# Optimization experiments

Measured on AMD Instinct MI355X. Metric: run time of the kernel, lower is better.

The kernel has to match this reference:

```python
import jax, jax.numpy as jnp
import numpy as np

B, IN, H = 4096, 1024, 2048


def setup_inputs() -> dict:
    key = jax.random.key(0)
    ks = jax.random.split(key, 7)
    return {
        "x": jax.random.normal(ks[0], (B, IN), jnp.float32),
        "h": jax.random.normal(ks[1], (B, H), jnp.float32),
        "c": jax.random.normal(ks[2], (B, H), jnp.float32),
        "w_ih": jax.random.normal(ks[3], (4 * H, IN), jnp.float32) * 0.02,
        "w_hh": jax.random.normal(ks[4], (4 * H, H), jnp.float32) * 0.02,
        "b_ih": jax.random.normal(ks[5], (4 * H,), jnp.float32) * 0.02,
        "b_hh": jax.random.normal(ks[6], (4 * H,), jnp.float32) * 0.02,
    }


def reference(x, h, c, w_ih, w_hh, b_ih, b_hh):
    act = jnp.sin  # custom gate activation (Sine_activation repo)
    # Combined GEMMs: same math as the 8 separate F.linear calls.
    # gates: [B, 4H], chunk order along dim 0 of weights: f, i, ic, o
    gates = (x @ w_ih.T + b_ih) + (h @ w_hh.T + b_hh)
    f_in, i_in, ic_in, o_in = jnp.split(gates, 4, axis=-1)
    ft = jax.nn.sigmoid(f_in)
    it = jax.nn.sigmoid(i_in)
    i_cands = act(ic_in)
    ct = c * ft + i_cands * it
    ot = jax.nn.sigmoid(o_in)
    ht = ot * act(ct)
    return (ht, ct)
```

## Files before the change

kernel.cpp:

```cpp
#include <hip/hip_runtime.h>

typedef __attribute__((ext_vector_type(8))) short short8;
typedef __attribute__((ext_vector_type(4))) float f32x4;

#define BDIM 4096
#define INDIM 1024
#define HDIM 2048
#define KDIM 3072
#define NDIM 8192
#define OUT_HALF 8388608
#define NKT 96
#define ACHUNKS 1572864

__device__ __forceinline__ unsigned short f2bf(float f) {
  unsigned u = __float_as_uint(f);
  u += 0x7FFFu + ((u >> 16) & 1u);
  return (unsigned short)(u >> 16);
}

__device__ __forceinline__ float sigmoidf_(float x) {
  return 1.0f / (1.0f + __expf(-x));
}

__global__ __launch_bounds__(256) void pack_all(
    const float* __restrict__ x, const float* __restrict__ hh,
    const float* __restrict__ w_ih, const float* __restrict__ w_hh,
    const float* __restrict__ b_ih, const float* __restrict__ b_hh,
    unsigned short* __restrict__ A, unsigned short* __restrict__ W,
    float* __restrict__ bias) {
  int idx = blockIdx.x * 256 + threadIdx.x;
  if (idx < ACHUNKS) {
    int m = idx / 384;
    int k0 = (idx - m * 384) * 8;
    const float* src = (k0 < INDIM) ? (x + (size_t)m * INDIM + k0)
                                    : (hh + (size_t)m * HDIM + (k0 - INDIM));
    float4 lo = ((const float4*)src)[0];
    float4 hi = ((const float4*)src)[1];
    union { unsigned short us[8]; uint4 v; } o;
    o.us[0] = f2bf(lo.x); o.us[1] = f2bf(lo.y); o.us[2] = f2bf(lo.z); o.us[3] = f2bf(lo.w);
    o.us[4] = f2bf(hi.x); o.us[5] = f2bf(hi.y); o.us[6] = f2bf(hi.z); o.us[7] = f2bf(hi.w);
    *(uint4*)(A + (size_t)m * KDIM + k0) = o.v;
  } else {
    idx -= ACHUNKS;
    int np = idx / 384;
    int rem = idx - np * 384;
    int k0 = rem * 8;
    int j = np >> 2;
    int g = np & 3;
    int n = g * HDIM + j;
    const float* src = (k0 < INDIM) ? (w_ih + (size_t)n * INDIM + k0)
                                    : (w_hh + (size_t)n * HDIM + (k0 - INDIM));
    float4 lo = ((const float4*)src)[0];
    float4 hi = ((const float4*)src)[1];
    union { unsigned short us[8]; uint4 v; } o;
    o.us[0] = f2bf(lo.x); o.us[1] = f2bf(lo.y); o.us[2] = f2bf(lo.z); o.us[3] = f2bf(lo.w);
    o.us[4] = f2bf(hi.x); o.us[5] = f2bf(hi.y); o.us[6] = f2bf(hi.z); o.us[7] = f2bf(hi.w);
    *(uint4*)(W + (size_t)np * KDIM + k0) = o.v;
    if (rem == 0) bias[np] = b_ih[n] + b_hh[n];
  }
}

__device__ __forceinline__ void gload_lds16(const void* g, void* l) {
  __builtin_amdgcn_global_load_lds(
      (const __attribute__((address_space(1))) void*)g,
      (__attribute__((address_space(3))) void*)l, 16, 0, 0);
}

#define SB0 __builtin_amdgcn_sched_barrier(0)

__global__ __launch_bounds__(512, 2) void lstm_gemm(
    const unsigned short* __restrict__ A,
    const unsigned short* __restrict__ W,
    const float* __restrict__ bias,
    const float* __restrict__ c,
    float* __restrict__ out) {
  extern __shared__ char smem[];

  const int tid = threadIdx.x;
  const int lane = tid & 63;
  const int wid = tid >> 6;

  const int bid = blockIdx.x;
  const int local = bid >> 3;
  const int tm = (bid & 7) * 2 + (local & 1);
  const int tn = local >> 1;

  int rowA0, clA0, rowA1, clA1;
  {
    int P0 = wid * 1024 + lane * 16;
    int P1 = 8192 + wid * 1024 + lane * 16;
    int r2, cp, cg;
    r2 = P0 >> 7; cp = (P0 >> 4) & 7; cg = cp ^ (r2 & 7);
    rowA0 = r2 * 2 + (cg >> 2); clA0 = cg & 3;
    r2 = P1 >> 7; cp = (P1 >> 4) & 7; cg = cp ^ (r2 & 7);
    rowA1 = r2 * 2 + (cg >> 2); clA1 = cg & 3;
  }
  const unsigned short* gA0 = A + (size_t)(tm * 256 + rowA0) * KDIM + clA0 * 8;
  const unsigned short* gA1 = A + (size_t)(tm * 256 + rowA1) * KDIM + clA1 * 8;
  const unsigned short* gB0 = W + (size_t)(tn * 256 + rowA0) * KDIM + clA0 * 8;
  const unsigned short* gB1 = W + (size_t)(tn * 256 + rowA1) * KDIM + clA1 * 8;
  const int ldA0 = wid * 1024;
  const int ldA1 = 8192 + wid * 1024;
  const int ldB0 = 16384 + wid * 1024;
  const int ldB1 = 24576 + wid * 1024;

  const int fr = lane & 15;
  const int fq = lane >> 4;
  const int wr = wid >> 2;
  const int wc = wid & 3;
  const int frh = fr >> 1;
  const int clA = (((fr & 1) << 2) | fq) ^ frh;
  const int aconst = wr * 8192 + frh * 128 + clA * 16;
  const int bconst = 16384 + wc * 4096 + frh * 128 + clA * 16;

  f32x4 acc[8][4] = {};
  short8 af[4], bf_[4], ag[4];

#pragma unroll
  for (int tt = 0; tt < 3; ++tt) {
    char* lb = smem + tt * 32768;
    gload_lds16(gA0, lb + ldA0);
    gload_lds16(gA1, lb + ldA1);
    gload_lds16(gB0, lb + ldB0);
    gload_lds16(gB1, lb + ldB1);
    gA0 += 32; gA1 += 32; gB0 += 32; gB1 += 32;
  }
  asm volatile("s_waitcnt vmcnt(8)" ::: "memory");
  __builtin_amdgcn_s_barrier(); SB0;
#pragma unroll
  for (int mi = 0; mi < 4; ++mi)
    af[mi] = *(const short8*)(smem + aconst + mi * 1024);
#pragma unroll
  for (int ni = 0; ni < 4; ++ni)
    bf_[ni] = *(const short8*)(smem + bconst + ni * 1024);

#define TILE_BODY(T, VMSTR, STAGE_, PREF_)                                   \
  do {                                                                       \
    const char* rb = smem + ((T) & 3) * 32768;                               \
    const char* rbn = smem + (((T) + 1) & 3) * 32768;                        \
    char* lb = smem + (((T) + 3) & 3) * 32768;                               \
    if (STAGE_) {                                                            \
      gload_lds16(gA0, lb + ldA0);                                           \
      gload_lds16(gA1, lb + ldA1);                                           \
    }                                                                        \
    _Pragma("unroll")                                                        \
    for (int mi = 0; mi < 4; ++mi)                                           \
      ag[mi] = *(const short8*)(rb + aconst + (mi + 4) * 1024);              \
    SB0;                                                                     \
    __builtin_amdgcn_s_setprio(1);                                           \
    _Pragma("unroll")                                                        \
    for (int mi = 0; mi < 4; ++mi)                                           \
      _Pragma("unroll")                                                      \
      for (int ni = 0; ni < 4; ++ni)                                         \
        acc[mi][ni] = __builtin_amdgcn_mfma_f32_16x16x32_bf16(               \
            af[mi], bf_[ni], acc[mi][ni], 0, 0, 0);                          \
    __builtin_amdgcn_s_setprio(0);                                           \
    if (STAGE_) {                                                            \
      gload_lds16(gB0, lb + ldB0);                                           \
      gload_lds16(gB1, lb + ldB1);                                           \
      gA0 += 32; gA1 += 32; gB0 += 32; gB1 += 32;                            \
    }                                                                        \
    asm volatile("s_waitcnt vmcnt(" VMSTR ")" ::: "memory");                 \
    asm volatile("s_waitcnt lgkmcnt(0)" ::: "memory");                       \
    __builtin_amdgcn_s_barrier(); SB0;                                       \
    if (PREF_) {                                                             \
      _Pragma("unroll")                                                      \
      for (int mi = 0; mi < 4; ++mi)                                         \
        af[mi] = *(const short8*)(rbn + aconst + mi * 1024);                 \
    }                                                                        \
    SB0;                                                                     \
    __builtin_amdgcn_s_setprio(1);                                           \
    _Pragma("unroll")                                                        \
    for (int mi = 0; mi < 4; ++mi)                                           \
      _Pragma("unroll")                                                      \
      for (int ni = 0; ni < 4; ++ni)                                         \
        acc[mi + 4][ni] = __builtin_amdgcn_mfma_f32_16x16x32_bf16(           \
            ag[mi], bf_[ni], acc[mi + 4][ni], 0, 0, 0);                      \
    __builtin_amdgcn_s_setprio(0);                                           \
    if (PREF_) {                                                             \
      _Pragma("unroll")                                                      \
      for (int ni = 0; ni < 4; ++ni)                                         \
        bf_[ni] = *(const short8*)(rbn + bconst + ni * 1024);                \
    }                                                                        \
  } while (0)

  for (int t = 0; t < NKT - 3; ++t) TILE_BODY(t, "8", true, true);
  TILE_BODY(NKT - 3, "4", false, true);
  TILE_BODY(NKT - 2, "0", false, true);
  TILE_BODY(NKT - 1, "0", false, false);
#undef TILE_BODY

  const int jw = fr;
  const int jg = tn * 64 + wc * 16 + jw;
  const f32x4 bi = *(const f32x4*)(bias + tn * 256 + wc * 64 + jw * 4);
  float* ep = (float*)smem + wid * 1152;

#pragma unroll
  for (int mi = 0; mi < 8; ++mi) {
#pragma unroll
    for (int ni = 0; ni < 4; ++ni)
#pragma unroll
      for (int r = 0; r < 4; ++r)
        ep[(fq * 4 + r) * 68 + ni * 16 + fr] = acc[mi][ni][r];
    asm volatile("s_waitcnt lgkmcnt(0)" ::: "memory");
#pragma unroll
    for (int t4 = 0; t4 < 4; ++t4) {
      const int row = fq + t4 * 4;
      f32x4 g4 = *(const f32x4*)(ep + row * 68 + jw * 4);
      const float f_in = g4[0] + bi[0];
      const float i_in = g4[1] + bi[1];
      const float ic_in = g4[2] + bi[2];
      const float o_in = g4[3] + bi[3];
      const float ft = sigmoidf_(f_in);
      const float it = sigmoidf_(i_in);
      const float ics = __sinf(ic_in);
      const int mg = tm * 256 + wr * 128 + mi * 16 + row;
      const float cv = c[(size_t)mg * HDIM + jg];
      const float ct = cv * ft + ics * it;
      const float ot = sigmoidf_(o_in);
      const float ht = ot * __sinf(ct);
      out[(size_t)mg * HDIM + jg] = ht;
      out[OUT_HALF + (size_t)mg * HDIM + jg] = ct;
    }
    asm volatile("s_waitcnt lgkmcnt(0)" ::: "memory");
  }
}

extern "C" void kernel_launch(void* const* d_in, const int* in_sizes, int n_in,
                              void* d_out, int out_size, void* d_ws, size_t ws_size,
                              hipStream_t stream) {
  const float* x    = (const float*)d_in[0];
  const float* h    = (const float*)d_in[1];
  const float* c    = (const float*)d_in[2];
  const float* w_ih = (const float*)d_in[3];
  const float* w_hh = (const float*)d_in[4];
  const float* b_ih = (const float*)d_in[5];
  const float* b_hh = (const float*)d_in[6];
  float* out = (float*)d_out;

  char* ws = (char*)d_ws;
  unsigned short* Abf = (unsigned short*)ws;
  unsigned short* Wbf = (unsigned short*)(ws + 25165824);
  float* bias = (float*)(ws + 25165824 + 50331648);

  hipFuncSetAttribute((const void*)lstm_gemm,
                      hipFuncAttributeMaxDynamicSharedMemorySize, 131072);

  pack_all<<<18432, 256, 0, stream>>>(x, h, w_ih, w_hh, b_ih, b_hh, Abf, Wbf, bias);
  lstm_gemm<<<512, 512, 131072, stream>>>(Abf, Wbf, bias, c, out);
}
```

Measured before the change: 219.2 us.

## Use 16 waves per block with 64x64 warp tiles in LSTM GEMM

Doubles the block to 1024 threads (16 waves in a 4x4 grid), so each wave computes a 64x64 sub-tile instead of 128x64. Each thread now issues one async global-to-LDS load per operand per K-tile, and the wait counts are adjusted to match. The aim is more waves to hide latency and lower per-thread register pressure. In exchange, each wave does fewer MFMAs per LDS fragment read, and barrier synchronisation among 16 waves costs more. The launch bounds of (1024, 4) ask for more resident waves than the 128 KB LDS per block probably allows.

New measurement: 221.0 us. About the same (+0.8%).

```diff
diff --git a/kernel.cpp b/kernel.cpp
--- a/kernel.cpp
+++ b/kernel.cpp
@@ -68,7 +68,7 @@
 
 #define SB0 __builtin_amdgcn_sched_barrier(0)
 
-__global__ __launch_bounds__(512, 2) void lstm_gemm(
+__global__ __launch_bounds__(1024, 4) void lstm_gemm(
     const unsigned short* __restrict__ A,
     const unsigned short* __restrict__ W,
     const float* __restrict__ bias,
@@ -85,51 +85,38 @@
   const int tm = (bid & 7) * 2 + (local & 1);
   const int tn = local >> 1;
 
-  int rowA0, clA0, rowA1, clA1;
-  {
-    int P0 = wid * 1024 + lane * 16;
-    int P1 = 8192 + wid * 1024 + lane * 16;
-    int r2, cp, cg;
-    r2 = P0 >> 7; cp = (P0 >> 4) & 7; cg = cp ^ (r2 & 7);
-    rowA0 = r2 * 2 + (cg >> 2); clA0 = cg & 3;
-    r2 = P1 >> 7; cp = (P1 >> 4) & 7; cg = cp ^ (r2 & 7);
-    rowA1 = r2 * 2 + (cg >> 2); clA1 = cg & 3;
-  }
-  const unsigned short* gA0 = A + (size_t)(tm * 256 + rowA0) * KDIM + clA0 * 8;
-  const unsigned short* gA1 = A + (size_t)(tm * 256 + rowA1) * KDIM + clA1 * 8;
-  const unsigned short* gB0 = W + (size_t)(tn * 256 + rowA0) * KDIM + clA0 * 8;
-  const unsigned short* gB1 = W + (size_t)(tn * 256 + rowA1) * KDIM + clA1 * 8;
-  const int ldA0 = wid * 1024;
-  const int ldA1 = 8192 + wid * 1024;
-  const int ldB0 = 16384 + wid * 1024;
-  const int ldB1 = 24576 + wid * 1024;
+  const int r2s = tid >> 3;
+  const int cgs = (tid & 7) ^ (r2s & 7);
+  const int srow = r2s * 2 + (cgs >> 2);
+  const int scol = (cgs & 3) * 8;
+  const unsigned short* gA = A + (size_t)(tm * 256 + srow) * KDIM + scol;
+  const unsigned short* gB = W + (size_t)(tn * 256 + srow) * KDIM + scol;
+  const int ldA = tid * 16;
+  const int ldB = 16384 + tid * 16;
 
   const int fr = lane & 15;
   const int fq = lane >> 4;
-  const int wr = wid >> 2;
-  const int wc = wid & 3;
+  const int wm = wid >> 2;
+  const int wn = wid & 3;
   const int frh = fr >> 1;
   const int clA = (((fr & 1) << 2) | fq) ^ frh;
-  const int aconst = wr * 8192 + frh * 128 + clA * 16;
-  const int bconst = 16384 + wc * 4096 + frh * 128 + clA * 16;
-
-  f32x4 acc[8][4] = {};
-  short8 af[4], bf_[4], ag[4];
+  const int aconst = wm * 4096 + frh * 128 + clA * 16;
+  const int bconst = 16384 + wn * 4096 + frh * 128 + clA * 16;
+
+  f32x4 acc[4][4] = {};
+  short8 af[4], bf_[4];
 
 #pragma unroll
   for (int tt = 0; tt < 3; ++tt) {
     char* lb = smem + tt * 32768;
-    gload_lds16(gA0, lb + ldA0);
-    gload_lds16(gA1, lb + ldA1);
-    gload_lds16(gB0, lb + ldB0);
-    gload_lds16(gB1, lb + ldB1);
-    gA0 += 32; gA1 += 32; gB0 += 32; gB1 += 32;
+    gload_lds16(gA, lb + ldA);
+    gload_lds16(gB, lb + ldB);
+    gA += 32; gB += 32;
   }
-  asm volatile("s_waitcnt vmcnt(8)" ::: "memory");
+  asm volatile("s_waitcnt vmcnt(4)" ::: "memory");
   __builtin_amdgcn_s_barrier(); SB0;
-#pragma unroll
-  for (int mi = 0; mi < 4; ++mi)
-    af[mi] = *(const short8*)(smem + aconst + mi * 1024);
+  af[0] = *(const short8*)(smem + aconst);
+  af[1] = *(const short8*)(smem + aconst + 1024);
 #pragma unroll
   for (int ni = 0; ni < 4; ++ni)
     bf_[ni] = *(const short8*)(smem + bconst + ni * 1024);
@@ -139,43 +126,37 @@
     const char* rb = smem + ((T) & 3) * 32768;                               \
     const char* rbn = smem + (((T) + 1) & 3) * 32768;                        \
     char* lb = smem + (((T) + 3) & 3) * 32768;                               \
-    if (STAGE_) {                                                            \
-      gload_lds16(gA0, lb + ldA0);                                           \
-      gload_lds16(gA1, lb + ldA1);                                           \
-    }                                                                        \
-    _Pragma("unroll")                                                        \
-    for (int mi = 0; mi < 4; ++mi)                                           \
-      ag[mi] = *(const short8*)(rb + aconst + (mi + 4) * 1024);              \
+    if (STAGE_) gload_lds16(gA, lb + ldA);                                   \
+    af[2] = *(const short8*)(rb + aconst + 2048);                            \
+    af[3] = *(const short8*)(rb + aconst + 3072);                            \
     SB0;                                                                     \
     __builtin_amdgcn_s_setprio(1);                                           \
     _Pragma("unroll")                                                        \
-    for (int mi = 0; mi < 4; ++mi)                                           \
+    for (int mi = 0; mi < 2; ++mi)                                           \
       _Pragma("unroll")                                                      \
       for (int ni = 0; ni < 4; ++ni)                                         \
         acc[mi][ni] = __builtin_amdgcn_mfma_f32_16x16x32_bf16(               \
             af[mi], bf_[ni], acc[mi][ni], 0, 0, 0);                          \
     __builtin_amdgcn_s_setprio(0);                                           \
     if (STAGE_) {                                                            \
-      gload_lds16(gB0, lb + ldB0);                                           \
-      gload_lds16(gB1, lb + ldB1);                                           \
-      gA0 += 32; gA1 += 32; gB0 += 32; gB1 += 32;                            \
+      gload_lds16(gB, lb + ldB);                                             \
+      gA += 32; gB += 32;                                                    \
     }                                                                        \
     asm volatile("s_waitcnt vmcnt(" VMSTR ")" ::: "memory");                 \
     asm volatile("s_waitcnt lgkmcnt(0)" ::: "memory");                       \
     __builtin_amdgcn_s_barrier(); SB0;                                       \
     if (PREF_) {                                                             \
-      _Pragma("unroll")                                                      \
-      for (int mi = 0; mi < 4; ++mi)                                         \
-        af[mi] = *(const short8*)(rbn + aconst + mi * 1024);                 \
+      af[0] = *(const short8*)(rbn + aconst);                                \
+      af[1] = *(const short8*)(rbn + aconst + 1024);                         \
     }                                                                        \
     SB0;                                                                     \
     __builtin_amdgcn_s_setprio(1);                                           \
     _Pragma("unroll")                                                        \
-    for (int mi = 0; mi < 4; ++mi)                                           \
+    for (int mi = 2; mi < 4; ++mi)                                           \
       _Pragma("unroll")                                                      \
       for (int ni = 0; ni < 4; ++ni)                                         \
-        acc[mi + 4][ni] = __builtin_amdgcn_mfma_f32_16x16x32_bf16(           \
-            ag[mi], bf_[ni], acc[mi + 4][ni], 0, 0, 0);                      \
+        acc[mi][ni] = __builtin_amdgcn_mfma_f32_16x16x32_bf16(               \
+            af[mi], bf_[ni], acc[mi][ni], 0, 0, 0);                          \
     __builtin_amdgcn_s_setprio(0);                                           \
     if (PREF_) {                                                             \
       _Pragma("unroll")                                                      \
@@ -184,19 +165,19 @@
     }                                                                        \
   } while (0)
 
-  for (int t = 0; t < NKT - 3; ++t) TILE_BODY(t, "8", true, true);
-  TILE_BODY(NKT - 3, "4", false, true);
+  for (int t = 0; t < NKT - 3; ++t) TILE_BODY(t, "4", true, true);
+  TILE_BODY(NKT - 3, "2", false, true);
   TILE_BODY(NKT - 2, "0", false, true);
   TILE_BODY(NKT - 1, "0", false, false);
 #undef TILE_BODY
 
   const int jw = fr;
-  const int jg = tn * 64 + wc * 16 + jw;
-  const f32x4 bi = *(const f32x4*)(bias + tn * 256 + wc * 64 + jw * 4);
+  const int jg = tn * 64 + wn * 16 + jw;
+  const f32x4 bi = *(const f32x4*)(bias + tn * 256 + wn * 64 + jw * 4);
   float* ep = (float*)smem + wid * 1152;
 
 #pragma unroll
-  for (int mi = 0; mi < 8; ++mi) {
+  for (int mi = 0; mi < 4; ++mi) {
 #pragma unroll
     for (int ni = 0; ni < 4; ++ni)
 #pragma unroll
@@ -214,7 +195,7 @@
       const float ft = sigmoidf_(f_in);
       const float it = sigmoidf_(i_in);
       const float ics = __sinf(ic_in);
-      const int mg = tm * 256 + wr * 128 + mi * 16 + row;
+      const int mg = tm * 256 + wm * 64 + mi * 16 + row;
       const float cv = c[(size_t)mg * HDIM + jg];
       const float ct = cv * ft + ics * it;
       const float ot = sigmoidf_(o_in);
@@ -247,5 +228,5 @@
                       hipFuncAttributeMaxDynamicSharedMemorySize, 131072);
 
   pack_all<<<18432, 256, 0, stream>>>(x, h, w_ih, w_hh, b_ih, b_hh, Abf, Wbf, bias);
-  lstm_gemm<<<512, 512, 131072, stream>>>(Abf, Wbf, bias, c, out);
-}
+  lstm_gemm<<<512, 1024, 131072, stream>>>(Abf, Wbf, bias, c, out);
+}
```
